# Kernel tuning notes

Measured on AMD Instinct MI355X. Metric: run time of the kernel, lower is better.

The kernel has to match this reference:

```python
import jax, jax.numpy as jnp
import numpy as np

B, D, O = 512, 256, 256
H = [512, 1024, 1024]

def _linear_params(key, fan_in, fan_out):
    kw, kb = jax.random.split(key)
    bound = 1.0 / np.sqrt(fan_in)
    W = jax.random.uniform(kw, (fan_out, fan_in), jnp.float32, -bound, bound)
    b = jax.random.uniform(kb, (fan_out,), jnp.float32, -bound, bound)
    return W, b

def setup_inputs() -> dict:
    key = jax.random.key(0)
    ks = jax.random.split(key, 7)
    input_values = jax.random.normal(ks[0], (B, D), jnp.float32)
    nan_flag = jax.random.uniform(ks[1], (B, D), jnp.float32)
    W_in, b_in = _linear_params(ks[2], D, H[0])          # input_layer: nan_flag_dim -> H[0]
    W_h1, b_h1 = _linear_params(ks[3], H[0], H[1])        # hidden layer 1
    W_h2, b_h2 = _linear_params(ks[4], H[1], H[2])        # hidden layer 2
    W_d, b_d = _linear_params(ks[5], H[2], D * O)         # output_branch_dense
    W_b, b_b = _linear_params(ks[6], H[2], O)             # output_branch_bias
    return {"input_values": input_values, "nan_flag": nan_flag, "training": False,
            "W_in": W_in, "b_in": b_in, "W_h1": W_h1, "b_h1": b_h1,
            "W_h2": W_h2, "b_h2": b_h2, "W_d": W_d, "b_d": b_d,
            "W_b": W_b, "b_b": b_b}

def reference(input_values, nan_flag, training, W_in, b_in, W_h1, b_h1, W_h2, b_h2, W_d, b_d, W_b, b_b):
    # training=False: dropout is identity, sample_missing branch skipped (default False)
    x = jax.nn.relu(nan_flag @ W_in.T + b_in)
    x = jax.nn.relu(x @ W_h1.T + b_h1)
    x = jax.nn.relu(x @ W_h2.T + b_h2)
    # per-sample compensation weights [B, D, O] and bias [B, O]
    comp_w = (x @ W_d.T + b_d).reshape(B, D, O)
    comp_b = x @ W_b.T + b_b
    # baddbmm: [B,1,D] @ [B,D,O] + [B,1,O] -> squeeze -> [B,O]
    out = comp_b + jnp.einsum('bd,bdo->bo', input_values, comp_w)
    return out
```

## Files before the change

### kernel.cpp

```cpp
#include <hip/hip_runtime.h>
#include <hip/hip_bf16.h>

#define B_  512
#define D_  256
#define O_  256
#define H2_ 1024

typedef __attribute__((ext_vector_type(4))) float    f32x4;
typedef __attribute__((ext_vector_type(8))) short    short8;
typedef __attribute__((ext_vector_type(4))) short    short4v;
typedef __attribute__((ext_vector_type(8))) _Float16 half8;

union S8u  { short4v v; unsigned u[2]; };
union H8u  { half8 v; short8 s; };

__device__ __forceinline__ unsigned f32_bf16(float x) {
  unsigned u = __builtin_bit_cast(unsigned, x);
  return (u + 0x7fffu + ((u >> 16) & 1u)) >> 16;
}
__device__ __forceinline__ unsigned cvt_pk_bf16(float a, float b) {
  return f32_bf16(a) | (f32_bf16(b) << 16);
}

__device__ __forceinline__ void gl_lds16(const void* g, void* l) {
  __builtin_amdgcn_global_load_lds(
      (const __attribute__((address_space(1))) unsigned int*)g,
      (__attribute__((address_space(3))) unsigned int*)l, 16, 0, 0);
}

__global__ __launch_bounds__(256)
void wcvt_h(const float* __restrict__ src, _Float16* __restrict__ dst, int n8) {
  int i = blockIdx.x * 256 + threadIdx.x;
  const int stride = gridDim.x * 256;
  for (; i < n8; i += stride) {
    const f32x4* p = (const f32x4*)(src + (size_t)i * 8);
    f32x4 a = p[0], b = p[1];
    half8 h;
    h[0] = (_Float16)a.x; h[1] = (_Float16)a.y; h[2] = (_Float16)a.z; h[3] = (_Float16)a.w;
    h[4] = (_Float16)b.x; h[5] = (_Float16)b.y; h[6] = (_Float16)b.z; h[7] = (_Float16)b.w;
    *(half8*)(dst + (size_t)i * 8) = h;
  }
}

template <int RELU>
__global__ __launch_bounds__(256)
void gemm_bt64(const float* __restrict__ A, const float* __restrict__ Bm,
               const float* __restrict__ bias, float* __restrict__ C,
               int M, int N, int K) {
  __shared__ __align__(16) short As[64][72];
  __shared__ __align__(16) short Bs[64][72];
  const int t    = threadIdx.x;
  const int m0   = blockIdx.y * 64;
  const int n0   = blockIdx.x * 64;
  const int f4c  = t & 15;
  const int rg   = t >> 4;
  const int lane = t & 63;
  const int w    = t >> 6;
  const int wm   = (w & 1) * 32;
  const int wn   = (w >> 1) * 32;
  const int lr   = lane & 15;
  const int lq   = lane >> 4;

  f32x4 acc[2][2];
  #pragma unroll
  for (int i = 0; i < 2; ++i)
    #pragma unroll
    for (int j = 0; j < 2; ++j) acc[i][j] = f32x4{0.f, 0.f, 0.f, 0.f};

  for (int k0 = 0; k0 < K; k0 += 64) {
    #pragma unroll
    for (int j = 0; j < 4; ++j) {
      int r = rg + 16 * j;
      f32x4 av = *(const f32x4*)(A  + (size_t)(m0 + r) * K + k0 + f4c * 4);
      f32x4 bv = *(const f32x4*)(Bm + (size_t)(n0 + r) * K + k0 + f4c * 4);
      S8u sa; sa.u[0] = cvt_pk_bf16(av.x, av.y); sa.u[1] = cvt_pk_bf16(av.z, av.w);
      S8u sb; sb.u[0] = cvt_pk_bf16(bv.x, bv.y); sb.u[1] = cvt_pk_bf16(bv.z, bv.w);
      *(short4v*)&As[r][f4c * 4] = sa.v;
      *(short4v*)&Bs[r][f4c * 4] = sb.v;
    }
    __syncthreads();
    #pragma unroll
    for (int ks = 0; ks < 2; ++ks) {
      short8 a0 = *(const short8*)&As[wm + lr     ][ks * 32 + lq * 8];
      short8 a1 = *(const short8*)&As[wm + 16 + lr][ks * 32 + lq * 8];
      short8 b0 = *(const short8*)&Bs[wn + lr     ][ks * 32 + lq * 8];
      short8 b1 = *(const short8*)&Bs[wn + 16 + lr][ks * 32 + lq * 8];
      acc[0][0] = __builtin_amdgcn_mfma_f32_16x16x32_bf16(a0, b0, acc[0][0], 0, 0, 0);
      acc[0][1] = __builtin_amdgcn_mfma_f32_16x16x32_bf16(a0, b1, acc[0][1], 0, 0, 0);
      acc[1][0] = __builtin_amdgcn_mfma_f32_16x16x32_bf16(a1, b0, acc[1][0], 0, 0, 0);
      acc[1][1] = __builtin_amdgcn_mfma_f32_16x16x32_bf16(a1, b1, acc[1][1], 0, 0, 0);
    }
    __syncthreads();
  }
  #pragma unroll
  for (int mi = 0; mi < 2; ++mi)
    #pragma unroll
    for (int ni = 0; ni < 2; ++ni)
      #pragma unroll
      for (int r = 0; r < 4; ++r) {
        int row = m0 + wm + mi * 16 + lq * 4 + r;
        int col = n0 + wn + ni * 16 + lr;
        float v = acc[mi][ni][r] + bias[col];
        if (RELU) v = fmaxf(v, 0.f);
        C[(size_t)row * N + col] = v;
      }
}

__global__ __launch_bounds__(256)
void bias_d_kernel(const float* __restrict__ inp, const float* __restrict__ b_d,
                   float* __restrict__ out) {
  const int b = blockIdx.x;
  const int o = threadIdx.x;
  const float* ir = inp + (size_t)b * D_;
  float s = 0.f;
  #pragma unroll 8
  for (int d = 0; d < D_; ++d)
    s += ir[d] * b_d[(size_t)d * O_ + o];
  out[(size_t)b * O_ + o] += s;
}

__global__ __launch_bounds__(256)
void stage_b6(const _Float16* __restrict__ x2h, const float* __restrict__ inp,
              const _Float16* __restrict__ Wdh, float* __restrict__ out) {
  __shared__ __align__(16) ushort As[128 * 64];
  __shared__ __align__(16) ushort Bs[128 * 64];
  const int t    = threadIdx.x;
  const int mt   = blockIdx.x >> 1;
  const int nt   = blockIdx.x & 1;
  const int d0   = blockIdx.y * 4;
  const int bm   = mt * 128;
  const int bn   = nt * 128;
  const int lane = t & 63;
  const int w    = t >> 6;
  const int wm   = (w & 1) * 64;
  const int wn   = (w >> 1) * 64;
  const int lr   = lane & 15;
  const int lq   = lane >> 4;
  const int srow = t >> 3;
  const int skc  = (t & 7) ^ ((t >> 3) & 7);

  f32x4 acc[4][4];
  #pragma unroll
  for (int mi = 0; mi < 4; ++mi)
    #pragma unroll
    for (int ni = 0; ni < 4; ++ni) acc[mi][ni] = f32x4{0.f, 0.f, 0.f, 0.f};

  const _Float16* xa = x2h + (size_t)bm * H2_;

  for (int dl = 0; dl < 4; ++dl) {
    const int d = d0 + dl;
    const _Float16* wb = Wdh + ((size_t)d * O_ + bn) * H2_;
    _Float16 hs[4];
    #pragma unroll
    for (int mi = 0; mi < 4; ++mi)
      hs[mi] = (_Float16)inp[(size_t)(bm + wm + mi * 16 + lr) * D_ + d];

    for (int h0 = 0; h0 < H2_; h0 += 64) {
      #pragma unroll
      for (int r = 0; r < 4; ++r) {
        int n = r * 32 + srow;
        gl_lds16(xa + (size_t)n * H2_ + h0 + skc * 8, &As[(size_t)(r * 256 + t) * 8]);
        gl_lds16(wb + (size_t)n * H2_ + h0 + skc * 8, &Bs[(size_t)(r * 256 + t) * 8]);
      }
      __syncthreads();
      #pragma unroll
      for (int ks = 0; ks < 2; ++ks) {
        half8 af[4], bfr[4];
        #pragma unroll
        for (int mi = 0; mi < 4; ++mi) {
          int m  = wm + mi * 16 + lr;
          int kc = (ks * 4 + lq) ^ (lr & 7);
          af[mi] = *(const half8*)&As[(size_t)(m * 8 + kc) * 8];
        }
        #pragma unroll
        for (int ni = 0; ni < 4; ++ni) {
          int n  = wn + ni * 16 + lr;
          int kc = (ks * 4 + lq) ^ (lr & 7);
          bfr[ni] = *(const half8*)&Bs[(size_t)(n * 8 + kc) * 8];
        }
        #pragma unroll
        for (int mi = 0; mi < 4; ++mi) {
          half8 asb = af[mi] * hs[mi];
          #pragma unroll
          for (int ni = 0; ni < 4; ++ni)
            acc[mi][ni] = __builtin_amdgcn_mfma_f32_16x16x32_f16(asb, bfr[ni],
                                                                 acc[mi][ni], 0, 0, 0);
        }
      }
      __syncthreads();
    }
  }

  #pragma unroll
  for (int mi = 0; mi < 4; ++mi)
    #pragma unroll
    for (int ni = 0; ni < 4; ++ni)
      #pragma unroll
      for (int r = 0; r < 4; ++r) {
        int row = bm + wm + mi * 16 + lq * 4 + r;
        int col = bn + wn + ni * 16 + lr;
        atomicAdd(out + (size_t)row * O_ + col, acc[mi][ni][r]);
      }
}

__global__ __launch_bounds__(256, 2)
void stage_b(const float* __restrict__ x2, const float* __restrict__ inp,
             const float* __restrict__ Wd, float* __restrict__ out) {
  __shared__ __align__(16) short As[128][72];
  __shared__ __align__(16) short Bs[128][72];
  const int t    = threadIdx.x;
  const int mt   = blockIdx.x >> 1;
  const int nt   = blockIdx.x & 1;
  const int d0   = blockIdx.y * 4;
  const int bm   = mt * 128;
  const int bn   = nt * 128;
  const int f4c  = t & 15;
  const int rg   = t >> 4;
  const int lane = t & 63;
  const int w    = t >> 6;
  const int wm   = (w & 1) * 64;
  const int wn   = (w >> 1) * 64;
  const int lr   = lane & 15;
  const int lq   = lane >> 4;

  f32x4 acc[4][4];
  #pragma unroll
  for (int mi = 0; mi < 4; ++mi)
    #pragma unroll
    for (int ni = 0; ni < 4; ++ni) acc[mi][ni] = f32x4{0.f, 0.f, 0.f, 0.f};

  for (int dl = 0; dl < 4; ++dl) {
    const int d = d0 + dl;
    float insc[8];
    #pragma unroll
    for (int j = 0; j < 8; ++j)
      insc[j] = inp[(size_t)(bm + rg + 16 * j) * D_ + d];
    const float* wbase = Wd + ((size_t)d * O_ + bn) * H2_;

    for (int h0 = 0; h0 < H2_; h0 += 64) {
      #pragma unroll
      for (int j = 0; j < 8; ++j) {
        int r = rg + 16 * j;
        f32x4 xv = *(const f32x4*)(x2 + (size_t)(bm + r) * H2_ + h0 + f4c * 4);
        float s = insc[j];
        S8u sa;
        sa.u[0] = cvt_pk_bf16(xv.x * s, xv.y * s);
        sa.u[1] = cvt_pk_bf16(xv.z * s, xv.w * s);
        *(short4v*)&As[r][f4c * 4] = sa.v;
        f32x4 wv = *(const f32x4*)(wbase + (size_t)r * H2_ + h0 + f4c * 4);
        S8u sb; sb.u[0] = cvt_pk_bf16(wv.x, wv.y); sb.u[1] = cvt_pk_bf16(wv.z, wv.w);
        *(short4v*)&Bs[r][f4c * 4] = sb.v;
      }
      __syncthreads();
      #pragma unroll
      for (int ks = 0; ks < 2; ++ks) {
        short8 af[4], bfr[4];
        #pragma unroll
        for (int mi = 0; mi < 4; ++mi)
          af[mi] = *(const short8*)&As[wm + mi * 16 + lr][ks * 32 + lq * 8];
        #pragma unroll
        for (int ni = 0; ni < 4; ++ni)
          bfr[ni] = *(const short8*)&Bs[wn + ni * 16 + lr][ks * 32 + lq * 8];
        #pragma unroll
        for (int mi = 0; mi < 4; ++mi)
          #pragma unroll
          for (int ni = 0; ni < 4; ++ni)
            acc[mi][ni] = __builtin_amdgcn_mfma_f32_16x16x32_bf16(af[mi], bfr[ni],
                                                                  acc[mi][ni], 0, 0, 0);
      }
      __syncthreads();
    }
  }

  #pragma unroll
  for (int mi = 0; mi < 4; ++mi)
    #pragma unroll
    for (int ni = 0; ni < 4; ++ni)
      #pragma unroll
      for (int r = 0; r < 4; ++r) {
        int row = bm + wm + mi * 16 + lq * 4 + r;
        int col = bn + wn + ni * 16 + lr;
        atomicAdd(out + (size_t)row * O_ + col, acc[mi][ni][r]);
      }
}

extern "C" void kernel_launch(void* const* d_in, const int* in_sizes, int n_in,
                              void* d_out, int out_size, void* d_ws, size_t ws_size,
                              hipStream_t stream) {
  const float* input = (const float*)d_in[0];
  const float* nanf  = (const float*)d_in[1];
  const float* W_in  = (const float*)d_in[3];
  const float* b_in  = (const float*)d_in[4];
  const float* W_h1  = (const float*)d_in[5];
  const float* b_h1  = (const float*)d_in[6];
  const float* W_h2  = (const float*)d_in[7];
  const float* b_h2  = (const float*)d_in[8];
  const float* W_d   = (const float*)d_in[9];
  const float* b_d   = (const float*)d_in[10];
  const float* W_b   = (const float*)d_in[11];
  const float* b_b   = (const float*)d_in[12];
  float* out = (float*)d_out;

  float* x0 = (float*)d_ws;
  float* x1 = x0 + 512 * 512;
  float* x2 = x1 + 512 * 1024;
  _Float16* Wdh = (_Float16*)(x2 + 512 * 1024);
  _Float16* x2h = Wdh + (size_t)65536 * 1024;
  const size_t need = 5242880 + ((size_t)65536 * 1024 + 512 * 1024) * 2;
  const bool use_f16 = ws_size >= need;

  if (use_f16)
    wcvt_h<<<8192, 256, 0, stream>>>(W_d, Wdh, 65536 * 1024 / 8);

  gemm_bt64<1><<<dim3(8, 8),  256, 0, stream>>>(nanf, W_in, b_in, x0, 512, 512, 256);
  gemm_bt64<1><<<dim3(16, 8), 256, 0, stream>>>(x0, W_h1, b_h1, x1, 512, 1024, 512);
  gemm_bt64<1><<<dim3(16, 8), 256, 0, stream>>>(x1, W_h2, b_h2, x2, 512, 1024, 1024);
  gemm_bt64<0><<<dim3(4, 8),  256, 0, stream>>>(x2, W_b, b_b, out, 512, 256, 1024);
  bias_d_kernel<<<512, 256, 0, stream>>>(input, b_d, out);

  if (use_f16) {
    wcvt_h<<<256, 256, 0, stream>>>(x2, x2h, 512 * 1024 / 8);
    stage_b6<<<dim3(8, 64), 256, 0, stream>>>(x2h, input, Wdh, out);
  } else {
    stage_b<<<dim3(8, 64), 256, 0, stream>>>(x2, input, W_d, out);
  }
}
```

Baseline: 640.8 us.

## Double-buffer LDS tiles in stage_b kernel to overlap loads with MFMA

The main compensation-weight GEMM kernel now uses two LDS buffers and a flattened loop over the d and h iterations. It issues global-to-LDS loads for the next tile before computing on the current one, with a single barrier per iteration instead of two. The aim is to hide global memory latency behind MFMA work. In exchange, LDS use doubles to 64KB per block, which may lower occupancy.

```diff
diff --git a/kernel.cpp b/kernel.cpp
--- a/kernel.cpp
+++ b/kernel.cpp
@@ -12,7 +12,6 @@
 typedef __attribute__((ext_vector_type(8))) _Float16 half8;
 
 union S8u  { short4v v; unsigned u[2]; };
-union H8u  { half8 v; short8 s; };
 
 __device__ __forceinline__ unsigned f32_bf16(float x) {
   unsigned u = __builtin_bit_cast(unsigned, x);
@@ -120,10 +119,10 @@
 }
 
 __global__ __launch_bounds__(256)
-void stage_b6(const _Float16* __restrict__ x2h, const float* __restrict__ inp,
+void stage_b7(const _Float16* __restrict__ x2h, const float* __restrict__ inp,
               const _Float16* __restrict__ Wdh, float* __restrict__ out) {
-  __shared__ __align__(16) ushort As[128 * 64];
-  __shared__ __align__(16) ushort Bs[128 * 64];
+  __shared__ __align__(16) ushort As[2][128 * 64];
+  __shared__ __align__(16) ushort Bs[2][128 * 64];
   const int t    = threadIdx.x;
   const int mt   = blockIdx.x >> 1;
   const int nt   = blockIdx.x & 1;
@@ -147,47 +146,63 @@
 
   const _Float16* xa = x2h + (size_t)bm * H2_;
 
-  for (int dl = 0; dl < 4; ++dl) {
-    const int d = d0 + dl;
-    const _Float16* wb = Wdh + ((size_t)d * O_ + bn) * H2_;
-    _Float16 hs[4];
-    #pragma unroll
-    for (int mi = 0; mi < 4; ++mi)
-      hs[mi] = (_Float16)inp[(size_t)(bm + wm + mi * 16 + lr) * D_ + d];
-
-    for (int h0 = 0; h0 < H2_; h0 += 64) {
+  {
+    const _Float16* wb = Wdh + ((size_t)d0 * O_ + bn) * H2_;
+    #pragma unroll
+    for (int r = 0; r < 4; ++r) {
+      int n = r * 32 + srow;
+      gl_lds16(xa + (size_t)n * H2_ + skc * 8, &As[0][(size_t)(r * 256 + t) * 8]);
+      gl_lds16(wb + (size_t)n * H2_ + skc * 8, &Bs[0][(size_t)(r * 256 + t) * 8]);
+    }
+  }
+
+  _Float16 hs[4];
+  for (int it = 0; it < 64; ++it) {
+    const int p  = it & 1;
+    if ((it & 15) == 0) {
+      const int d = d0 + (it >> 4);
+      #pragma unroll
+      for (int mi = 0; mi < 4; ++mi)
+        hs[mi] = (_Float16)inp[(size_t)(bm + wm + mi * 16 + lr) * D_ + d];
+    }
+    __syncthreads();
+    if (it < 63) {
+      const int itn = it + 1;
+      const int dn  = d0 + (itn >> 4);
+      const int hn  = (itn & 15) * 64;
+      const _Float16* wbn = Wdh + ((size_t)dn * O_ + bn) * H2_;
       #pragma unroll
       for (int r = 0; r < 4; ++r) {
         int n = r * 32 + srow;
-        gl_lds16(xa + (size_t)n * H2_ + h0 + skc * 8, &As[(size_t)(r * 256 + t) * 8]);
-        gl_lds16(wb + (size_t)n * H2_ + h0 + skc * 8, &Bs[(size_t)(r * 256 + t) * 8]);
-      }
-      __syncthreads();
-      #pragma unroll
-      for (int ks = 0; ks < 2; ++ks) {
-        half8 af[4], bfr[4];
+        gl_lds16(xa  + (size_t)n * H2_ + hn + skc * 8,
+                 &As[1 - p][(size_t)(r * 256 + t) * 8]);
+        gl_lds16(wbn + (size_t)n * H2_ + hn + skc * 8,
+                 &Bs[1 - p][(size_t)(r * 256 + t) * 8]);
+      }
+    }
+    #pragma unroll
+    for (int ks = 0; ks < 2; ++ks) {
+      half8 af[4], bfr[4];
+      #pragma unroll
+      for (int mi = 0; mi < 4; ++mi) {
+        int m  = wm + mi * 16 + lr;
+        int kc = (ks * 4 + lq) ^ (lr & 7);
+        af[mi] = *(const half8*)&As[p][(size_t)(m * 8 + kc) * 8];
+      }
+      #pragma unroll
+      for (int ni = 0; ni < 4; ++ni) {
+        int n  = wn + ni * 16 + lr;
+        int kc = (ks * 4 + lq) ^ (lr & 7);
+        bfr[ni] = *(const half8*)&Bs[p][(size_t)(n * 8 + kc) * 8];
+      }
+      #pragma unroll
+      for (int mi = 0; mi < 4; ++mi) {
+        half8 asb = af[mi] * hs[mi];
         #pragma unroll
-        for (int mi = 0; mi < 4; ++mi) {
-          int m  = wm + mi * 16 + lr;
-          int kc = (ks * 4 + lq) ^ (lr & 7);
-          af[mi] = *(const half8*)&As[(size_t)(m * 8 + kc) * 8];
-        }
-        #pragma unroll
-        for (int ni = 0; ni < 4; ++ni) {
-          int n  = wn + ni * 16 + lr;
-          int kc = (ks * 4 + lq) ^ (lr & 7);
-          bfr[ni] = *(const half8*)&Bs[(size_t)(n * 8 + kc) * 8];
-        }
-        #pragma unroll
-        for (int mi = 0; mi < 4; ++mi) {
-          half8 asb = af[mi] * hs[mi];
-          #pragma unroll
-          for (int ni = 0; ni < 4; ++ni)
-            acc[mi][ni] = __builtin_amdgcn_mfma_f32_16x16x32_f16(asb, bfr[ni],
-                                                                 acc[mi][ni], 0, 0, 0);
-        }
-      }
-      __syncthreads();
+        for (int ni = 0; ni < 4; ++ni)
+          acc[mi][ni] = __builtin_amdgcn_mfma_f32_16x16x32_f16(asb, bfr[ni],
+                                                               acc[mi][ni], 0, 0, 0);
+      }
     }
   }
 
@@ -320,7 +335,7 @@
 
   if (use_f16) {
     wcvt_h<<<256, 256, 0, stream>>>(x2, x2h, 512 * 1024 / 8);
-    stage_b6<<<dim3(8, 64), 256, 0, stream>>>(x2h, input, Wdh, out);
+    stage_b7<<<dim3(8, 64), 256, 0, stream>>>(x2h, input, Wdh, out);
   } else {
     stage_b<<<dim3(8, 64), 256, 0, stream>>>(x2, input, W_d, out);
   }
```

Measured after the change: 637.6 us. No clear change (-0.5%).
